# Kernel tuning notes

Hardware: AMD Instinct MI355X
Metric: run time of the kernel (lower is better)

The kernel has to match this reference:

```python
import jax, jax.numpy as jnp
import numpy as np

D_MODEL = 1024
N_REG = 8
D_REG = 32
LN_EPS = 1e-5


def setup_inputs() -> dict:
    key = jax.random.key(0)
    ks = jax.random.split(key, 14)
    s = 0.02
    return {
        "x": jax.random.normal(ks[0], (8, 2048, D_MODEL), dtype=jnp.float32),
        "ln_w": jnp.ones((D_MODEL,), jnp.float32),
        "ln_b": jnp.zeros((D_MODEL,), jnp.float32),
        "Wrq": jax.random.normal(ks[1], (N_REG, D_MODEL), jnp.float32) * s,
        "brq": jax.random.normal(ks[2], (N_REG,), jnp.float32) * s,
        "Wrp": jax.random.normal(ks[3], (D_MODEL, D_REG), jnp.float32) * s,
        "brp": jax.random.normal(ks[4], (D_MODEL,), jnp.float32) * s,
        "Wwq": jax.random.normal(ks[5], (N_REG, D_MODEL), jnp.float32) * s,
        "bwq": jax.random.normal(ks[6], (N_REG,), jnp.float32) * s,
        "Wwv": jax.random.normal(ks[7], (D_REG, D_MODEL), jnp.float32) * s,
        "bwv": jax.random.normal(ks[8], (D_REG,), jnp.float32) * s,
        "Wwg": jax.random.normal(ks[9], (1, D_MODEL), jnp.float32) * s,
        "bwg": jnp.full((1,), -3.0, jnp.float32),
        "mix": jnp.asarray(0.001, jnp.float32),
    }


def _layernorm(x, w, b):
    mu = jnp.mean(x, axis=-1, keepdims=True)
    var = jnp.mean(jnp.square(x - mu), axis=-1, keepdims=True)
    return (x - mu) * jax.lax.rsqrt(var + LN_EPS) * w + b


def _forward(x, ln_w, ln_b, Wrq, brq, Wrp, brp, Wwq, bwq, Wwv, bwv, Wwg, bwg, mix):
    B, L, D = x.shape
    h = _layernorm(x, ln_w, ln_b)  # (B,L,D)
    # Precompute all per-timestep projections as big GEMMs (same math as per-step Linear)
    r_w = jax.nn.softmax(jnp.einsum("bld,rd->blr", h, Wrq) + brq, axis=-1)  # (B,L,R)
    w_w = jax.nn.softmax(jnp.einsum("bld,rd->blr", h, Wwq) + bwq, axis=-1)  # (B,L,R)
    w_v = jnp.einsum("bld,kd->blk", h, Wwv) + bwv                           # (B,L,Dr)
    w_g = jax.nn.sigmoid(jnp.einsum("bld,od->blo", h, Wwg) + bwg)           # (B,L,1)

    def step(registers, inputs):
        rw_t, ww_t, wv_t, wg_t = inputs  # (B,R), (B,R), (B,Dr), (B,1)
        r_v = jnp.einsum("br,brd->bd", rw_t, registers)  # read (B,Dr)
        us = (ww_t * wg_t)[..., None]                     # (B,R,1)
        new_regs = (1.0 - us) * registers + us * wv_t[:, None, :]
        return new_regs, r_v

    init_regs = jnp.zeros((B, N_REG, D_REG), x.dtype)
    seq = (
        jnp.moveaxis(r_w, 1, 0),
        jnp.moveaxis(w_w, 1, 0),
        jnp.moveaxis(w_v, 1, 0),
        jnp.moveaxis(w_g, 1, 0),
    )
    _, r_vs = jax.lax.scan(step, init_regs, seq)  # (L,B,Dr)
    r_vs = jnp.moveaxis(r_vs, 0, 1)               # (B,L,Dr)
    r_out = jnp.einsum("blk,dk->bld", r_vs, Wrp) + brp  # read_proj
    return mix * r_out


def reference(x, ln_w, ln_b, Wrq, brq, Wrp, brp, Wwq, bwq, Wwv, bwv, Wwg, bwg, mix):
    return _forward(x, ln_w, ln_b, Wrq, brq, Wrp, brp, Wwq, bwq, Wwv, bwv, Wwg, bwg, mix)
```

## Files before the change

kernel.cpp:

```cpp
#include <hip/hip_runtime.h>

#define D_MODEL 1024
#define L_SEQ   2048
#define N_BATCH 8
#define N_TOK   (N_BATCH * L_SEQ)
#define N_REGS  8
#define D_REG   32
#define LN_EPS  1e-5f

#define KC      32
#define XSTR    65
#define XQ      (KC * XSTR)
#define SSTR    57

#define HSTEP   16
#define N_HALF  128

__device__ __forceinline__ float wred(float v) {
    #pragma unroll
    for (int off = 32; off > 0; off >>= 1) v += __shfl_xor(v, off, 64);
    return v;
}

__device__ __forceinline__ float sigmoidf(float z) {
    return 1.f / (1.f + expf(-z));
}

__global__ __launch_bounds__(256) void k_prep(
    const float* __restrict__ ln_w, const float* __restrict__ ln_b,
    const float* __restrict__ Wrq,  const float* __restrict__ brq,
    const float* __restrict__ Wwq,  const float* __restrict__ bwq,
    const float* __restrict__ Wwv,  const float* __restrict__ bwv,
    const float* __restrict__ Wwg,  const float* __restrict__ bwg,
    float* __restrict__ Wpp, float* __restrict__ c1, float* __restrict__ c2)
{
    const int f = blockIdx.x;
    const int g = f / 13, i = f % 13;

    const float* wrow = nullptr; float bias = 0.f;
    if (f < 8)        { wrow = Wrq + f * D_MODEL;        bias = brq[f]; }
    else if (f < 16)  { wrow = Wwq + (f - 8) * D_MODEL;  bias = bwq[f - 8]; }
    else if (f == 16) { wrow = Wwg;                      bias = bwg[0]; }
    else if (f < 49)  { wrow = Wwv + (f - 17) * D_MODEL; bias = bwv[f - 17]; }

    float p1 = 0.f, p2 = 0.f;
    #pragma unroll
    for (int j = 0; j < 4; ++j) {
        const int k = j * 256 + threadIdx.x;
        float w  = wrow ? wrow[k] : 0.f;
        float wg = w * ln_w[k];
        Wpp[((size_t)(g * D_MODEL + k)) * 16 + i] = wg;
        p1 += wg;
        p2 = fmaf(w, ln_b[k], p2);
    }
    p1 = wred(p1); p2 = wred(p2);

    __shared__ float r1[4], r2[4];
    const int l = threadIdx.x & 63, w = threadIdx.x >> 6;
    if (l == 0) { r1[w] = p1; r2[w] = p2; }
    __syncthreads();
    if (threadIdx.x == 0) {
        c1[f] = r1[0] + r1[1] + r1[2] + r1[3];
        c2[f] = r2[0] + r2[1] + r2[2] + r2[3] + bias;
    }
}

template<int STATS>
__device__ __forceinline__ void proj_chunk(
    const float* __restrict__ lx,
    const float4* __restrict__ wr0,
    int lane, float acc[13], float& st)
{
    #pragma unroll 4
    for (int k = 0; k < KC; ++k) {
        const float xs = lx[k * XSTR + lane];
        const float4* wr = wr0 + (k << 2);
        float4 wa = wr[0], wb = wr[1], wc = wr[2];
        float  wd = reinterpret_cast<const float*>(wr)[12];
        acc[0]  = fmaf(xs, wa.x, acc[0]);
        acc[1]  = fmaf(xs, wa.y, acc[1]);
        acc[2]  = fmaf(xs, wa.z, acc[2]);
        acc[3]  = fmaf(xs, wa.w, acc[3]);
        acc[4]  = fmaf(xs, wb.x, acc[4]);
        acc[5]  = fmaf(xs, wb.y, acc[5]);
        acc[6]  = fmaf(xs, wb.z, acc[6]);
        acc[7]  = fmaf(xs, wb.w, acc[7]);
        acc[8]  = fmaf(xs, wc.x, acc[8]);
        acc[9]  = fmaf(xs, wc.y, acc[9]);
        acc[10] = fmaf(xs, wc.z, acc[10]);
        acc[11] = fmaf(xs, wc.w, acc[11]);
        acc[12] = fmaf(xs, wd,   acc[12]);
        if (STATS == 1) st += xs;
        if (STATS == 2) st = fmaf(xs, xs, st);
    }
}

__global__ __launch_bounds__(1024) void k_lnproj3(
    const float* __restrict__ x,
    const float* __restrict__ Wpp,
    const float* __restrict__ c1, const float* __restrict__ c2,
    float* __restrict__ rw_o, float* __restrict__ us_o, float* __restrict__ wv_o)
{
    extern __shared__ float lds[];
    float* Sb = lds + 2 * 4 * XQ;

    const int tid  = threadIdx.x;
    const int lane = tid & 63;
    const int wv   = tid >> 6;
    const int g    = wv & 3;
    const int kh   = wv >> 2;
    const int tok0 = blockIdx.x * 64;

    const int gs  = __builtin_amdgcn_readfirstlane(g);
    const int khs = __builtin_amdgcn_readfirstlane(kh);

    const int tq  = tid & 255;
    const int row = tq >> 3;
    const int c4  = tq & 7;

    const float4* x4 = reinterpret_cast<const float4*>(x);

    float4 xg[2];
    float acc[13];
    #pragma unroll
    for (int i = 0; i < 13; ++i) acc[i] = 0.f;
    float st = 0.f;

    const size_t gbase = (size_t)(tok0 + row) * 256 + khs * 64 + c4;

    {
        xg[0] = x4[gbase];
        xg[1] = x4[gbase + 32 * 256];
        float* dst = lds + khs * XQ + (c4 * 4) * XSTR;
        #pragma unroll
        for (int p = 0; p < 2; ++p) {
            const int r = row + 32 * p;
            dst[0 * XSTR + r] = xg[p].x;
            dst[1 * XSTR + r] = xg[p].y;
            dst[2 * XSTR + r] = xg[p].z;
            dst[3 * XSTR + r] = xg[p].w;
        }
    }
    __syncthreads();

    for (int c = 0; c < 8; ++c) {
        if (c < 7)  {
            xg[0] = x4[gbase + (size_t)(c + 1) * 8];
            xg[1] = x4[gbase + (size_t)(c + 1) * 8 + 32 * 256];
        }

        const float*  lx  = lds + ((c & 1) * 4 + khs) * XQ;
        const float4* wr0 = reinterpret_cast<const float4*>(Wpp)
                          + ((gs * D_MODEL + khs * 256 + c * KC) << 2);
        if (gs == 1)      proj_chunk<1>(lx, wr0, lane, acc, st);
        else if (gs == 2) proj_chunk<2>(lx, wr0, lane, acc, st);
        else              proj_chunk<0>(lx, wr0, lane, acc, st);

        if (c < 7) {
            float* dst = lds + (((c + 1) & 1) * 4 + khs) * XQ + (c4 * 4) * XSTR;
            #pragma unroll
            for (int p = 0; p < 2; ++p) {
                const int r = row + 32 * p;
                dst[0 * XSTR + r] = xg[p].x;
                dst[1 * XSTR + r] = xg[p].y;
                dst[2 * XSTR + r] = xg[p].z;
                dst[3 * XSTR + r] = xg[p].w;
            }
        }
        __syncthreads();
    }

    if (kh == 0) {
        #pragma unroll
        for (int i = 0; i < 13; ++i) Sb[lane * SSTR + g * 13 + i] = acc[i];
        if (g == 1) Sb[lane * SSTR + 52] = st;
        if (g == 2) Sb[lane * SSTR + 53] = st;
    }
    __syncthreads();
    #pragma unroll
    for (int ph = 1; ph < 4; ++ph) {
        if (kh == ph) {
            #pragma unroll
            for (int i = 0; i < 13; ++i) Sb[lane * SSTR + g * 13 + i] += acc[i];
            if (g == 1) Sb[lane * SSTR + 52] += st;
            if (g == 2) Sb[lane * SSTR + 53] += st;
        }
        __syncthreads();
    }

    if (tid < 256) {
        const int t  = tid & 63;
        const int q  = tid >> 6;
        const int tg = blockIdx.x * 64 + t;
        const float* St = Sb + t * SSTR;

        const float tsum = St[52], tss = St[53];
        const float mu  = tsum * (1.f / D_MODEL);
        const float var = tss * (1.f / D_MODEL) - mu * mu;
        const float rs  = rsqrtf(var + LN_EPS);

        if (q == 0) {
            float lg[8];
            #pragma unroll
            for (int r = 0; r < 8; ++r)
                lg[r] = rs * (St[r] - mu * c1[r]) + c2[r];
            float m = lg[0];
            #pragma unroll
            for (int r = 1; r < 8; ++r) m = fmaxf(m, lg[r]);
            float sm = 0.f;
            #pragma unroll
            for (int r = 0; r < 8; ++r) { lg[r] = expf(lg[r] - m); sm += lg[r]; }
            float inv = 1.f / sm;
            float4* o = reinterpret_cast<float4*>(rw_o + (size_t)tg * 8);
            o[0] = make_float4(lg[0]*inv, lg[1]*inv, lg[2]*inv, lg[3]*inv);
            o[1] = make_float4(lg[4]*inv, lg[5]*inv, lg[6]*inv, lg[7]*inv);
        } else if (q == 1) {
            float lg[8];
            #pragma unroll
            for (int r = 0; r < 8; ++r)
                lg[r] = rs * (St[8 + r] - mu * c1[8 + r]) + c2[8 + r];
            float gl = rs * (St[16] - mu * c1[16]) + c2[16];
            float m = lg[0];
            #pragma unroll
            for (int r = 1; r < 8; ++r) m = fmaxf(m, lg[r]);
            float sm = 0.f;
            #pragma unroll
            for (int r = 0; r < 8; ++r) { lg[r] = expf(lg[r] - m); sm += lg[r]; }
            float inv = sigmoidf(gl) / sm;
            float4* o = reinterpret_cast<float4*>(us_o + (size_t)tg * 8);
            o[0] = make_float4(lg[0]*inv, lg[1]*inv, lg[2]*inv, lg[3]*inv);
            o[1] = make_float4(lg[4]*inv, lg[5]*inv, lg[6]*inv, lg[7]*inv);
        } else {
            const int f0 = 17 + (q - 2) * 16;
            float4* o = reinterpret_cast<float4*>(wv_o + (size_t)tg * 32 + (q - 2) * 16);
            #pragma unroll
            for (int jq = 0; jq < 4; ++jq) {
                float v0 = rs * (St[f0 + jq*4 + 0] - mu * c1[f0 + jq*4 + 0]) + c2[f0 + jq*4 + 0];
                float v1 = rs * (St[f0 + jq*4 + 1] - mu * c1[f0 + jq*4 + 1]) + c2[f0 + jq*4 + 1];
                float v2 = rs * (St[f0 + jq*4 + 2] - mu * c1[f0 + jq*4 + 2]) + c2[f0 + jq*4 + 2];
                float v3 = rs * (St[f0 + jq*4 + 3] - mu * c1[f0 + jq*4 + 3]) + c2[f0 + jq*4 + 3];
                o[jq] = make_float4(v0, v1, v2, v3);
            }
        }
    }
}

__global__ __launch_bounds__(1024) void k_scan(
    const float* __restrict__ us, const float* __restrict__ wv,
    float* __restrict__ S0)
{
    __shared__ float S_us[L_SEQ];
    __shared__ float lA[N_HALF];
    __shared__ float lB[N_HALF * 32];

    const int tid = threadIdx.x;
    const int b   = blockIdx.x >> 3;
    const int r   = blockIdx.x & 7;

    #pragma unroll
    for (int i = 0; i < 2; ++i) {
        const int t = i * 1024 + tid;
        S_us[t] = us[((size_t)(b * L_SEQ + t)) * 8 + r];
    }
    __syncthreads();

    const int k  = tid & 31;
    const int hb = (tid >> 5) * 4;
    #pragma unroll
    for (int j = 0; j < 4; ++j) {
        const int h  = hb + j;
        const int t0 = h * HSTEP;
        const float* wvp = wv + ((size_t)(b * L_SEQ + t0)) * 32 + k;

        float Aacc = 1.f, Bacc = 0.f;
        #pragma unroll
        for (int gq = 0; gq < 2; ++gq) {
            float wl[8], ul[8];
            #pragma unroll
            for (int e = 0; e < 8; ++e) {
                wl[e] = wvp[(gq * 8 + e) * 32];
                ul[e] = S_us[t0 + gq * 8 + e];
            }
            #pragma unroll
            for (int e = 0; e < 8; ++e) {
                float a = 1.f - ul[e];
                Aacc *= a;
                Bacc = fmaf(a, Bacc, ul[e] * wl[e]);
            }
        }
        lB[h * 32 + k] = Bacc;
        if (k == 0) lA[h] = Aacc;
    }
    __syncthreads();

    if (tid < 32) {
        float stv = 0.f;
        float* S0p = S0 + ((size_t)(b * 8 + r) * N_HALF) * 32 + tid;
        for (int h = 0; h < N_HALF; ++h) {
            S0p[h * 32] = stv;
            stv = fmaf(lA[h], stv, lB[h * 32 + tid]);
        }
    }
}

__global__ __launch_bounds__(256) void k_replay2(
    const float* __restrict__ rw, const float* __restrict__ us,
    const float* __restrict__ wv, const float* __restrict__ S0,
    float* __restrict__ rvs)
{
    const int gid = blockIdx.x * 256 + threadIdx.x;
    const int k   = gid & 31;
    const int hu  = gid >> 5;
    const int b   = hu >> 7;
    const int ch2 = hu & 127;

    float s[8];
    #pragma unroll
    for (int r = 0; r < 8; ++r)
        s[r] = S0[((size_t)((b * 8 + r) * N_HALF) + ch2) * 32 + k];

    const int t0 = b * L_SEQ + ch2 * HSTEP;
    const float* rwp = rw + (size_t)t0 * 8;
    const float* usp = us + (size_t)t0 * 8;
    const float* wvp = wv + (size_t)t0 * 32 + k;
    float*       rvp = rvs + (size_t)t0 * 32 + k;

    #pragma unroll
    for (int g4 = 0; g4 < 4; ++g4) {
        float4 r0[4], r1[4], u0[4], u1[4];
        float  wl[4];
        #pragma unroll
        for (int j = 0; j < 4; ++j) {
            const int t = g4 * 4 + j;
            r0[j] = reinterpret_cast<const float4*>(rwp + t * 8)[0];
            r1[j] = reinterpret_cast<const float4*>(rwp + t * 8)[1];
            u0[j] = reinterpret_cast<const float4*>(usp + t * 8)[0];
            u1[j] = reinterpret_cast<const float4*>(usp + t * 8)[1];
            wl[j] = wvp[t * 32];
        }
        #pragma unroll
        for (int j = 0; j < 4; ++j) {
            const int t = g4 * 4 + j;
            float rv = r0[j].x*s[0] + r0[j].y*s[1] + r0[j].z*s[2] + r0[j].w*s[3]
                     + r1[j].x*s[4] + r1[j].y*s[5] + r1[j].z*s[6] + r1[j].w*s[7];
            rvp[t * 32] = rv;
            const float w = wl[j];
            s[0] = fmaf(u0[j].x, w - s[0], s[0]);
            s[1] = fmaf(u0[j].y, w - s[1], s[1]);
            s[2] = fmaf(u0[j].z, w - s[2], s[2]);
            s[3] = fmaf(u0[j].w, w - s[3], s[3]);
            s[4] = fmaf(u1[j].x, w - s[4], s[4]);
            s[5] = fmaf(u1[j].y, w - s[5], s[5]);
            s[6] = fmaf(u1[j].z, w - s[6], s[6]);
            s[7] = fmaf(u1[j].w, w - s[7], s[7]);
        }
    }
}

__global__ __launch_bounds__(256) void k_outproj(
    const float* __restrict__ rvs, const float* __restrict__ Wrp,
    const float* __restrict__ brp, const float* __restrict__ mix_p,
    float* __restrict__ out)
{
    const int d    = blockIdx.y * 256 + threadIdx.x;
    const int tok0 = blockIdx.x * 64;

    float4 wr[8];
    #pragma unroll
    for (int q = 0; q < 8; ++q)
        wr[q] = reinterpret_cast<const float4*>(Wrp)[(size_t)d * 8 + q];

    const float bias = brp[d];
    const float mix  = mix_p[0];

    for (int t = 0; t < 64; ++t) {
        const float4* rv = reinterpret_cast<const float4*>(rvs + (size_t)(tok0 + t) * 32);
        float acc = 0.f;
        #pragma unroll
        for (int q = 0; q < 8; ++q) {
            float4 v = rv[q];
            acc += wr[q].x*v.x + wr[q].y*v.y + wr[q].z*v.z + wr[q].w*v.w;
        }
        out[(size_t)(tok0 + t) * D_MODEL + d] = mix * (acc + bias);
    }
}

extern "C" void kernel_launch(void* const* d_in, const int* in_sizes, int n_in,
                              void* d_out, int out_size, void* d_ws, size_t ws_size,
                              hipStream_t stream)
{
    const float* x    = (const float*)d_in[0];
    const float* ln_w = (const float*)d_in[1];
    const float* ln_b = (const float*)d_in[2];
    const float* Wrq  = (const float*)d_in[3];
    const float* brq  = (const float*)d_in[4];
    const float* Wrp  = (const float*)d_in[5];
    const float* brp  = (const float*)d_in[6];
    const float* Wwq  = (const float*)d_in[7];
    const float* bwq  = (const float*)d_in[8];
    const float* Wwv  = (const float*)d_in[9];
    const float* bwv  = (const float*)d_in[10];
    const float* Wwg  = (const float*)d_in[11];
    const float* bwg  = (const float*)d_in[12];
    const float* mix  = (const float*)d_in[13];
    float* out = (float*)d_out;

    float* ws   = (float*)d_ws;
    float* rw_b = ws;
    float* us_b = ws + 131072;
    float* wv_b = ws + 262144;
    float* S0_b = ws + 786432;
    float* rv_b = ws + 1048576;
    float* Wpp  = rv_b;
    float* c1_b = rv_b + 65536;
    float* c2_b = rv_b + 65600;

    const size_t lds_bytes = (size_t)(2 * 4 * XQ + 64 * SSTR) * 4;

    k_prep<<<52, 256, 0, stream>>>(ln_w, ln_b, Wrq, brq, Wwq, bwq,
                                   Wwv, bwv, Wwg, bwg, Wpp, c1_b, c2_b);
    k_lnproj3<<<256, 1024, lds_bytes, stream>>>(x, Wpp, c1_b, c2_b,
                                                rw_b, us_b, wv_b);
    k_scan   <<<64, 1024, 0, stream>>>(us_b, wv_b, S0_b);
    k_replay2<<<128, 256, 0, stream>>>(rw_b, us_b, wv_b, S0_b, rv_b);
    dim3 gc(N_TOK / 64, 4);
    k_outproj<<<gc, 256, 0, stream>>>(rv_b, Wrp, brp, mix, out);
}
```

Baseline: 84.22 us.

## Replace FP32 FMA layernorm-projection with split-bf16 MFMA GEMM

Rewrites the fused layernorm plus projection kernel to compute the 64-wide projection on matrix cores. Both activations and the prepacked weights are split into bf16 high and low parts, and three MFMA products recover near-fp32 accuracy. The weight prep now emits transposed bf16 hi/lo arrays, and the per-token sum and sum of squares are computed during conversion. The goal is to offload the scalar FMA work to MFMA units, at the cost of conversion overhead and a small loss of precision.

```diff
diff --git a/kernel.cpp b/kernel.cpp
--- a/kernel.cpp
+++ b/kernel.cpp
@@ -8,14 +8,26 @@
 #define D_REG   32
 #define LN_EPS  1e-5f
 
-#define KC      32
-#define XSTR    65
-#define XQ      (KC * XSTR)
-#define SSTR    57
-
 #define HSTEP   16
 #define N_HALF  128
 
+#define ASTR    36
+#define ABUF    (64 * ASTR)
+#define BUFSZ   (4 * ABUF)
+#define OFF_AH  0
+#define OFF_AL  ABUF
+#define OFF_BH  (2 * ABUF)
+#define OFF_BL  (3 * ABUF)
+#define OFF_SB  (2 * BUFSZ)
+#define SBSTR   68
+#define OFF_PH  (OFF_SB + 64 * SBSTR)
+#define OFF_PS  (OFF_PH + 64 * 17)
+#define LDS_DW  (OFF_PS + 64 * 17)
+
+typedef short short8v __attribute__((ext_vector_type(8)));
+typedef short short4v __attribute__((ext_vector_type(4)));
+typedef float float4v __attribute__((ext_vector_type(4)));
+
 __device__ __forceinline__ float wred(float v) {
     #pragma unroll
     for (int off = 32; off > 0; off >>= 1) v += __shfl_xor(v, off, 64);
@@ -26,16 +38,24 @@
     return 1.f / (1.f + expf(-z));
 }
 
-__global__ __launch_bounds__(256) void k_prep(
+__device__ __forceinline__ unsigned short f2bf(float f) {
+    unsigned u = __float_as_uint(f);
+    return (unsigned short)((u + 0x7FFFu + ((u >> 16) & 1u)) >> 16);
+}
+__device__ __forceinline__ float bf2f(unsigned short h) {
+    return __uint_as_float(((unsigned)h) << 16);
+}
+
+__global__ __launch_bounds__(256) void k_prep2(
     const float* __restrict__ ln_w, const float* __restrict__ ln_b,
     const float* __restrict__ Wrq,  const float* __restrict__ brq,
     const float* __restrict__ Wwq,  const float* __restrict__ bwq,
     const float* __restrict__ Wwv,  const float* __restrict__ bwv,
     const float* __restrict__ Wwg,  const float* __restrict__ bwg,
-    float* __restrict__ Wpp, float* __restrict__ c1, float* __restrict__ c2)
+    unsigned short* __restrict__ Wbh, unsigned short* __restrict__ Wbl,
+    float* __restrict__ c1, float* __restrict__ c2)
 {
     const int f = blockIdx.x;
-    const int g = f / 13, i = f % 13;
 
     const float* wrow = nullptr; float bias = 0.f;
     if (f < 8)        { wrow = Wrq + f * D_MODEL;        bias = brq[f]; }
@@ -48,9 +68,12 @@
     for (int j = 0; j < 4; ++j) {
         const int k = j * 256 + threadIdx.x;
         float w  = wrow ? wrow[k] : 0.f;
-        float wg = w * ln_w[k];
-        Wpp[((size_t)(g * D_MODEL + k)) * 16 + i] = wg;
-        p1 += wg;
+        float wp = w * ln_w[k];
+        unsigned short h = f2bf(wp);
+        unsigned short l = f2bf(wp - bf2f(h));
+        Wbh[(size_t)f * D_MODEL + k] = h;
+        Wbl[(size_t)f * D_MODEL + k] = l;
+        p1 += wp;
         p2 = fmaf(w, ln_b[k], p2);
     }
     p1 = wred(p1); p2 = wred(p2);
@@ -65,136 +88,113 @@
     }
 }
 
-template<int STATS>
-__device__ __forceinline__ void proj_chunk(
-    const float* __restrict__ lx,
-    const float4* __restrict__ wr0,
-    int lane, float acc[13], float& st)
-{
-    #pragma unroll 4
-    for (int k = 0; k < KC; ++k) {
-        const float xs = lx[k * XSTR + lane];
-        const float4* wr = wr0 + (k << 2);
-        float4 wa = wr[0], wb = wr[1], wc = wr[2];
-        float  wd = reinterpret_cast<const float*>(wr)[12];
-        acc[0]  = fmaf(xs, wa.x, acc[0]);
-        acc[1]  = fmaf(xs, wa.y, acc[1]);
-        acc[2]  = fmaf(xs, wa.z, acc[2]);
-        acc[3]  = fmaf(xs, wa.w, acc[3]);
-        acc[4]  = fmaf(xs, wb.x, acc[4]);
-        acc[5]  = fmaf(xs, wb.y, acc[5]);
-        acc[6]  = fmaf(xs, wb.z, acc[6]);
-        acc[7]  = fmaf(xs, wb.w, acc[7]);
-        acc[8]  = fmaf(xs, wc.x, acc[8]);
-        acc[9]  = fmaf(xs, wc.y, acc[9]);
-        acc[10] = fmaf(xs, wc.z, acc[10]);
-        acc[11] = fmaf(xs, wc.w, acc[11]);
-        acc[12] = fmaf(xs, wd,   acc[12]);
-        if (STATS == 1) st += xs;
-        if (STATS == 2) st = fmaf(xs, xs, st);
-    }
-}
-
-__global__ __launch_bounds__(1024) void k_lnproj3(
+__device__ __forceinline__ void cvt_write_a(
+    float* lds, int wb, int stok, int skq, float4 v, float& ssum, float& ssq)
+{
+    unsigned short h0 = f2bf(v.x), h1 = f2bf(v.y), h2 = f2bf(v.z), h3 = f2bf(v.w);
+    short4v hv, lv;
+    hv[0] = (short)h0; hv[1] = (short)h1; hv[2] = (short)h2; hv[3] = (short)h3;
+    lv[0] = (short)f2bf(v.x - bf2f(h0));
+    lv[1] = (short)f2bf(v.y - bf2f(h1));
+    lv[2] = (short)f2bf(v.z - bf2f(h2));
+    lv[3] = (short)f2bf(v.w - bf2f(h3));
+    *reinterpret_cast<short4v*>(lds + wb + OFF_AH + stok * ASTR + skq * 2) = hv;
+    *reinterpret_cast<short4v*>(lds + wb + OFF_AL + stok * ASTR + skq * 2) = lv;
+    ssum += v.x + v.y + v.z + v.w;
+    ssq = fmaf(v.x, v.x, fmaf(v.y, v.y, fmaf(v.z, v.z, fmaf(v.w, v.w, ssq))));
+}
+
+__global__ __launch_bounds__(1024) void k_lnmfma(
     const float* __restrict__ x,
-    const float* __restrict__ Wpp,
+    const uint4* __restrict__ Wbh, const uint4* __restrict__ Wbl,
     const float* __restrict__ c1, const float* __restrict__ c2,
     float* __restrict__ rw_o, float* __restrict__ us_o, float* __restrict__ wv_o)
 {
     extern __shared__ float lds[];
-    float* Sb = lds + 2 * 4 * XQ;
 
     const int tid  = threadIdx.x;
     const int lane = tid & 63;
     const int wv   = tid >> 6;
-    const int g    = wv & 3;
-    const int kh   = wv >> 2;
+    const int tt   = wv >> 2;
+    const int ft   = wv & 3;
     const int tok0 = blockIdx.x * 64;
 
-    const int gs  = __builtin_amdgcn_readfirstlane(g);
-    const int khs = __builtin_amdgcn_readfirstlane(kh);
-
-    const int tq  = tid & 255;
-    const int row = tq >> 3;
-    const int c4  = tq & 7;
-
-    const float4* x4 = reinterpret_cast<const float4*>(x);
-
-    float4 xg[2];
-    float acc[13];
-    #pragma unroll
-    for (int i = 0; i < 13; ++i) acc[i] = 0.f;
-    float st = 0.f;
-
-    const size_t gbase = (size_t)(tok0 + row) * 256 + khs * 64 + c4;
-
+    const int stok = tid >> 4;
+    const int skq  = tid & 15;
+    const float4* xg4 = reinterpret_cast<const float4*>(x) + (size_t)(tok0 + stok) * 256;
+    const uint4*  wsrc = (skq < 8 ? Wbh : Wbl) + (size_t)stok * 128;
+    const int     wkq  = skq & 7;
+    const int     wdst = (skq < 8 ? OFF_BH : OFF_BL) + stok * ASTR + wkq * 4;
+
+    float ssum = 0.f, ssq = 0.f;
+    float4 xg = xg4[skq];
+    uint4  bg = wsrc[wkq];
+
+    cvt_write_a(lds, 0, stok, skq, xg, ssum, ssq);
+    *reinterpret_cast<uint4*>(lds + wdst) = bg;
+    __syncthreads();
+
+    float4v acc = {0.f, 0.f, 0.f, 0.f};
+    const int m = lane & 15, oct = lane >> 4;
+    const int arow = (tt * 16 + m) * ASTR + oct * 4;
+    const int brow = (ft * 16 + m) * ASTR + oct * 4;
+
+    for (int c = 0; c < 16; ++c) {
+        if (c < 15) {
+            xg = xg4[(c + 1) * 16 + skq];
+            bg = wsrc[(c + 1) * 8 + wkq];
+        }
+        const int bb = (c & 1) * BUFSZ;
+        #pragma unroll
+        for (int ks = 0; ks < 2; ++ks) {
+            const int ao = bb + arow + ks * 16;
+            const int bo = bb + brow + ks * 16;
+            short8v ah = *reinterpret_cast<const short8v*>(lds + OFF_AH + ao);
+            short8v al = *reinterpret_cast<const short8v*>(lds + OFF_AL + ao);
+            short8v bh = *reinterpret_cast<const short8v*>(lds + OFF_BH + bo);
+            short8v bl = *reinterpret_cast<const short8v*>(lds + OFF_BL + bo);
+            acc = __builtin_amdgcn_mfma_f32_16x16x32_bf16(ah, bh, acc, 0, 0, 0);
+            acc = __builtin_amdgcn_mfma_f32_16x16x32_bf16(ah, bl, acc, 0, 0, 0);
+            acc = __builtin_amdgcn_mfma_f32_16x16x32_bf16(al, bh, acc, 0, 0, 0);
+        }
+        if (c < 15) {
+            const int wb = ((c + 1) & 1) * BUFSZ;
+            cvt_write_a(lds, wb, stok, skq, xg, ssum, ssq);
+            *reinterpret_cast<uint4*>(lds + wb + wdst) = bg;
+        }
+        __syncthreads();
+    }
+
+    lds[OFF_PH + stok * 17 + skq] = ssum;
+    lds[OFF_PS + stok * 17 + skq] = ssq;
     {
-        xg[0] = x4[gbase];
-        xg[1] = x4[gbase + 32 * 256];
-        float* dst = lds + khs * XQ + (c4 * 4) * XSTR;
-        #pragma unroll
-        for (int p = 0; p < 2; ++p) {
-            const int r = row + 32 * p;
-            dst[0 * XSTR + r] = xg[p].x;
-            dst[1 * XSTR + r] = xg[p].y;
-            dst[2 * XSTR + r] = xg[p].z;
-            dst[3 * XSTR + r] = xg[p].w;
-        }
-    }
-    __syncthreads();
-
-    for (int c = 0; c < 8; ++c) {
-        if (c < 7)  {
-            xg[0] = x4[gbase + (size_t)(c + 1) * 8];
-            xg[1] = x4[gbase + (size_t)(c + 1) * 8 + 32 * 256];
-        }
-
-        const float*  lx  = lds + ((c & 1) * 4 + khs) * XQ;
-        const float4* wr0 = reinterpret_cast<const float4*>(Wpp)
-                          + ((gs * D_MODEL + khs * 256 + c * KC) << 2);
-        if (gs == 1)      proj_chunk<1>(lx, wr0, lane, acc, st);
-        else if (gs == 2) proj_chunk<2>(lx, wr0, lane, acc, st);
-        else              proj_chunk<0>(lx, wr0, lane, acc, st);
-
-        if (c < 7) {
-            float* dst = lds + (((c + 1) & 1) * 4 + khs) * XQ + (c4 * 4) * XSTR;
-            #pragma unroll
-            for (int p = 0; p < 2; ++p) {
-                const int r = row + 32 * p;
-                dst[0 * XSTR + r] = xg[p].x;
-                dst[1 * XSTR + r] = xg[p].y;
-                dst[2 * XSTR + r] = xg[p].z;
-                dst[3 * XSTR + r] = xg[p].w;
-            }
-        }
-        __syncthreads();
-    }
-
-    if (kh == 0) {
-        #pragma unroll
-        for (int i = 0; i < 13; ++i) Sb[lane * SSTR + g * 13 + i] = acc[i];
-        if (g == 1) Sb[lane * SSTR + 52] = st;
-        if (g == 2) Sb[lane * SSTR + 53] = st;
-    }
-    __syncthreads();
-    #pragma unroll
-    for (int ph = 1; ph < 4; ++ph) {
-        if (kh == ph) {
-            #pragma unroll
-            for (int i = 0; i < 13; ++i) Sb[lane * SSTR + g * 13 + i] += acc[i];
-            if (g == 1) Sb[lane * SSTR + 52] += st;
-            if (g == 2) Sb[lane * SSTR + 53] += st;
-        }
-        __syncthreads();
-    }
+        const int row0 = tt * 16 + oct * 4;
+        const int col  = ft * 16 + m;
+        #pragma unroll
+        for (int r = 0; r < 4; ++r)
+            lds[OFF_SB + (row0 + r) * SBSTR + col] = acc[r];
+    }
+    __syncthreads();
+
+    if (tid < 64) {
+        float s = 0.f, q = 0.f;
+        #pragma unroll
+        for (int i = 0; i < 16; ++i) {
+            s += lds[OFF_PH + tid * 17 + i];
+            q += lds[OFF_PS + tid * 17 + i];
+        }
+        lds[OFF_SB + tid * SBSTR + 50] = s;
+        lds[OFF_SB + tid * SBSTR + 51] = q;
+    }
+    __syncthreads();
 
     if (tid < 256) {
         const int t  = tid & 63;
         const int q  = tid >> 6;
         const int tg = blockIdx.x * 64 + t;
-        const float* St = Sb + t * SSTR;
-
-        const float tsum = St[52], tss = St[53];
+        const float* St = lds + OFF_SB + t * SBSTR;
+
+        const float tsum = St[50], tss = St[51];
         const float mu  = tsum * (1.f / D_MODEL);
         const float var = tss * (1.f / D_MODEL) - mu * mu;
         const float rs  = rsqrtf(var + LN_EPS);
@@ -204,12 +204,12 @@
             #pragma unroll
             for (int r = 0; r < 8; ++r)
                 lg[r] = rs * (St[r] - mu * c1[r]) + c2[r];
-            float m = lg[0];
-            #pragma unroll
-            for (int r = 1; r < 8; ++r) m = fmaxf(m, lg[r]);
+            float mx = lg[0];
+            #pragma unroll
+            for (int r = 1; r < 8; ++r) mx = fmaxf(mx, lg[r]);
             float sm = 0.f;
             #pragma unroll
-            for (int r = 0; r < 8; ++r) { lg[r] = expf(lg[r] - m); sm += lg[r]; }
+            for (int r = 0; r < 8; ++r) { lg[r] = expf(lg[r] - mx); sm += lg[r]; }
             float inv = 1.f / sm;
             float4* o = reinterpret_cast<float4*>(rw_o + (size_t)tg * 8);
             o[0] = make_float4(lg[0]*inv, lg[1]*inv, lg[2]*inv, lg[3]*inv);
@@ -220,12 +220,12 @@
             for (int r = 0; r < 8; ++r)
                 lg[r] = rs * (St[8 + r] - mu * c1[8 + r]) + c2[8 + r];
             float gl = rs * (St[16] - mu * c1[16]) + c2[16];
-            float m = lg[0];
-            #pragma unroll
-            for (int r = 1; r < 8; ++r) m = fmaxf(m, lg[r]);
+            float mx = lg[0];
+            #pragma unroll
+            for (int r = 1; r < 8; ++r) mx = fmaxf(mx, lg[r]);
             float sm = 0.f;
             #pragma unroll
-            for (int r = 0; r < 8; ++r) { lg[r] = expf(lg[r] - m); sm += lg[r]; }
+            for (int r = 0; r < 8; ++r) { lg[r] = expf(lg[r] - mx); sm += lg[r]; }
             float inv = sigmoidf(gl) / sm;
             float4* o = reinterpret_cast<float4*>(us_o + (size_t)tg * 8);
             o[0] = make_float4(lg[0]*inv, lg[1]*inv, lg[2]*inv, lg[3]*inv);
@@ -411,16 +411,15 @@
     float* wv_b = ws + 262144;
     float* S0_b = ws + 786432;
     float* rv_b = ws + 1048576;
-    float* Wpp  = rv_b;
+    unsigned short* Wbh = (unsigned short*)rv_b;
+    unsigned short* Wbl = (unsigned short*)(rv_b + 32768);
     float* c1_b = rv_b + 65536;
     float* c2_b = rv_b + 65600;
 
-    const size_t lds_bytes = (size_t)(2 * 4 * XQ + 64 * SSTR) * 4;
-
-    k_prep<<<52, 256, 0, stream>>>(ln_w, ln_b, Wrq, brq, Wwq, bwq,
-                                   Wwv, bwv, Wwg, bwg, Wpp, c1_b, c2_b);
-    k_lnproj3<<<256, 1024, lds_bytes, stream>>>(x, Wpp, c1_b, c2_b,
-                                                rw_b, us_b, wv_b);
+    k_prep2<<<64, 256, 0, stream>>>(ln_w, ln_b, Wrq, brq, Wwq, bwq,
+                                    Wwv, bwv, Wwg, bwg, Wbh, Wbl, c1_b, c2_b);
+    k_lnmfma<<<256, 1024, LDS_DW * 4, stream>>>(
+        x, (const uint4*)Wbh, (const uint4*)Wbl, c1_b, c2_b, rw_b, us_b, wv_b);
     k_scan   <<<64, 1024, 0, stream>>>(us_b, wv_b, S0_b);
     k_replay2<<<128, 256, 0, stream>>>(rw_b, us_b, wv_b, S0_b, rv_b);
     dim3 gc(N_TOK / 64, 4);
```

After: 85.42 us. Within noise of the previous version (+1.4%).
